# Kernel tuning notes

Hardware: AMD Instinct MI355X
Metric: run time of the kernel (lower is better)

Reference implementation:

```python
import jax, jax.numpy as jnp
import numpy as np

BS = 128  # block size for gating tiles


def setup_inputs() -> dict:
    key = jax.random.key(0)
    k1, k2, k3 = jax.random.split(key, 3)
    batch, dim_in, dim_out = 1536, 1536, 4608
    X = jax.random.normal(k1, (batch, dim_in), dtype=jnp.float32)
    W = jax.random.normal(k2, (dim_in, dim_out), dtype=jnp.float32)
    G = jax.random.normal(k3, (batch, dim_in // BS, dim_out // BS), dtype=jnp.float32)
    return {"X": X, "W": W, "G": G}


def reference(X, W, G):
    # Block-gated matmul: Y[b, j] = sum_i X[b, i] * W[i, j] * G[b, i//BS, j//BS]
    B, DI = X.shape
    DO = W.shape[1]
    NI, NJ = DI // BS, DO // BS
    Xr = X.reshape(B, NI, BS)               # [B, NI, bs]
    Wr = W.reshape(NI, BS, NJ, BS)          # [NI, bs, NJ, bs]
    # per-input-block partial products gated by G, summed over input blocks
    Y = jnp.einsum('bik,ikjl,bij->bjl', Xr, Wr, G)  # [B, NJ, bs]
    s = Y.sum()
    return s * s
```

## Files before the change

### kernel.cpp

```cpp
#include <hip/hip_runtime.h>


#define B_DIM 1536
#define DI    1536
#define DO    4608
#define BS    128
#define NI    12
#define NJ    36
#define BTILE 16

__global__ __launch_bounds__(256) void wsum_kernel(const float* __restrict__ W,
                                                   float* __restrict__ Wsum) {
    int wave = (blockIdx.x * 256 + threadIdx.x) >> 6;
    int lane = threadIdx.x & 63;
    int i  = wave / NJ;
    int jb = wave % NJ;
    const float2* p = (const float2*)(W + (size_t)i * DO + (size_t)jb * BS);
    float2 v = p[lane];
    float s = v.x + v.y;
    #pragma unroll
    for (int off = 32; off > 0; off >>= 1)
        s += __shfl_down(s, off, 64);
    if (lane == 0) Wsum[wave] = s;
}

__global__ __launch_bounds__(256) void gated_kernel(const float* __restrict__ X,
                                                    const float* __restrict__ G,
                                                    const float* __restrict__ Wsum,
                                                    float* __restrict__ partials) {
    __shared__ float ws[BS * 37];
    __shared__ float gs[BTILE * NJ];
    __shared__ float red[4];

    const int ib   = blockIdx.x % NI;
    const int tile = blockIdx.x / NI;
    const int b0   = tile * BTILE;
    const int t    = threadIdx.x;

    const float* wbase = Wsum + (size_t)ib * BS * NJ;
    for (int e = t; e < BS * NJ; e += 256) {
        int r = e / NJ, c = e - r * NJ;
        ws[r * 37 + c] = wbase[e];
    }
    for (int e = t; e < BTILE * NJ; e += 256) {
        int bb = e / NJ, k = e - bb * NJ;
        gs[e] = G[((size_t)(b0 + bb) * NI + ib) * NJ + k];
    }
    __syncthreads();

    const int wave = t >> 6, lane = t & 63;
    float waveAcc = 0.f;
    for (int bb = wave; bb < BTILE; bb += 4) {
        const int b = b0 + bb;
        const float* xrow = X + (size_t)b * DI + (size_t)ib * BS;
        const float* grow = gs + bb * NJ;
        float p = 0.f;
        #pragma unroll
        for (int r = 0; r < 2; ++r) {
            const int il = lane + 64 * r;
            float x = xrow[il];
            float acc = 0.f;
            #pragma unroll
            for (int k = 0; k < NJ; ++k)
                acc += ws[il * 37 + k] * grow[k];
            p += x * acc;
        }
        #pragma unroll
        for (int off = 32; off > 0; off >>= 1)
            p += __shfl_down(p, off, 64);
        if (lane == 0) waveAcc += p;
    }
    if (lane == 0) red[wave] = waveAcc;
    __syncthreads();
    if (t == 0) partials[blockIdx.x] = red[0] + red[1] + red[2] + red[3];
}

__global__ __launch_bounds__(256) void finish_kernel(const float* __restrict__ partials,
                                                     int n, float* __restrict__ out) {
    __shared__ float red[4];
    const int t = threadIdx.x;
    float s = 0.f;
    for (int e = t; e < n; e += 256) s += partials[e];
    #pragma unroll
    for (int off = 32; off > 0; off >>= 1)
        s += __shfl_down(s, off, 64);
    const int wave = t >> 6, lane = t & 63;
    if (lane == 0) red[wave] = s;
    __syncthreads();
    if (t == 0) {
        float tot = red[0] + red[1] + red[2] + red[3];
        out[0] = tot * tot;
    }
}

extern "C" void kernel_launch(void* const* d_in, const int* in_sizes, int n_in,
                              void* d_out, int out_size, void* d_ws, size_t ws_size,
                              hipStream_t stream) {
    const float* X = (const float*)d_in[0];
    const float* W = (const float*)d_in[1];
    const float* G = (const float*)d_in[2];
    float* out = (float*)d_out;

    float* Wsum     = (float*)d_ws;
    float* partials = Wsum + (size_t)DI * NJ;
    const int n_partials = (B_DIM / BTILE) * NI;

    wsum_kernel<<<(DI * NJ) / 4, 256, 0, stream>>>(W, Wsum);
    gated_kernel<<<n_partials, 256, 0, stream>>>(X, G, Wsum, partials);
    finish_kernel<<<1, 256, 0, stream>>>(partials, n_partials, out);
}
```

Baseline: 97.03 us.

## Restructure gated reduction: accumulate X·G per input column, fuse finish via atomics

The gated kernel now gives each lane one input column and accumulates x·G over a 32-row batch range into 36 register accumulators. It dots those with the precomputed W block sums only at the end, instead of redoing the 36-term W·G dot product for every batch row out of shared memory. The separate finish kernel is replaced by atomicAdd on a global accumulator plus a last-block counter, which removes one launch. The W-sum kernel reads float4 so each wave handles two column blocks, and it also zeroes the accumulator. The atomic float sum makes the result order-nondeterministic, and the larger per-thread register footprint may lower occupancy.

```diff
diff --git a/kernel.cpp b/kernel.cpp
--- a/kernel.cpp
+++ b/kernel.cpp
@@ -4,92 +4,90 @@
 #define B_DIM 1536
 #define DI    1536
 #define DO    4608
-#define BS    128
 #define NI    12
 #define NJ    36
-#define BTILE 16
+#define GROW  (NI * NJ)
+#define K2_WAVES 1152
+#define K2_BLOCKS (K2_WAVES / 4)
 
 __global__ __launch_bounds__(256) void wsum_kernel(const float* __restrict__ W,
-                                                   float* __restrict__ Wsum) {
-    int wave = (blockIdx.x * 256 + threadIdx.x) >> 6;
+                                                   float* __restrict__ Wsum,
+                                                   float* __restrict__ acc,
+                                                   unsigned* __restrict__ counter) {
+    if (blockIdx.x == 0 && threadIdx.x == 0) { *acc = 0.f; *counter = 0u; }
+    int g    = blockIdx.x * 4 + (threadIdx.x >> 6);
     int lane = threadIdx.x & 63;
-    int i  = wave / NJ;
-    int jb = wave % NJ;
-    const float2* p = (const float2*)(W + (size_t)i * DO + (size_t)jb * BS);
-    float2 v = p[lane];
-    float s = v.x + v.y;
+    int i = g / 18;
+    int w = g - i * 18;
+    const float4* p = (const float4*)(W + (size_t)i * DO + (size_t)w * 256);
+    float4 v = p[lane];
+    float s = (v.x + v.y) + (v.z + v.w);
     #pragma unroll
-    for (int off = 32; off > 0; off >>= 1)
-        s += __shfl_down(s, off, 64);
-    if (lane == 0) Wsum[wave] = s;
+    for (int off = 16; off > 0; off >>= 1) s += __shfl_xor(s, off, 64);
+    if (lane == 0)  Wsum[i * NJ + 2 * w]     = s;
+    if (lane == 32) Wsum[i * NJ + 2 * w + 1] = s;
 }
 
 __global__ __launch_bounds__(256) void gated_kernel(const float* __restrict__ X,
                                                     const float* __restrict__ G,
                                                     const float* __restrict__ Wsum,
-                                                    float* __restrict__ partials) {
-    __shared__ float ws[BS * 37];
-    __shared__ float gs[BTILE * NJ];
+                                                    float* __restrict__ acc,
+                                                    unsigned* __restrict__ counter,
+                                                    float* __restrict__ out) {
     __shared__ float red[4];
+    const int t    = threadIdx.x;
+    const int w    = __builtin_amdgcn_readfirstlane(t >> 6);
+    const int lane = t & 63;
+    const int wave = blockIdx.x * 4 + w;
+    const int iblk = wave % 24;
+    const int brng = wave / 24;
+    const int b0   = brng * 32;
+    const int i    = iblk * 64 + lane;
+    const int ib   = iblk >> 1;
 
-    const int ib   = blockIdx.x % NI;
-    const int tile = blockIdx.x / NI;
-    const int b0   = tile * BTILE;
-    const int t    = threadIdx.x;
+    float acc36[NJ];
+    #pragma unroll
+    for (int k = 0; k < NJ; ++k) acc36[k] = 0.f;
 
-    const float* wbase = Wsum + (size_t)ib * BS * NJ;
-    for (int e = t; e < BS * NJ; e += 256) {
-        int r = e / NJ, c = e - r * NJ;
-        ws[r * 37 + c] = wbase[e];
+    const float* xp = X + (size_t)b0 * DI + i;
+    const float4* gp = (const float4*)(G + (size_t)b0 * GROW + (size_t)ib * NJ);
+    const int gstride4 = GROW / 4;
+
+    #pragma unroll 8
+    for (int bb = 0; bb < 32; ++bb) {
+        float x = xp[(size_t)bb * DI];
+        const float4* g4 = gp + (size_t)bb * gstride4;
+        #pragma unroll
+        for (int k4 = 0; k4 < 9; ++k4) {
+            float4 gv = g4[k4];
+            acc36[4*k4+0] = fmaf(x, gv.x, acc36[4*k4+0]);
+            acc36[4*k4+1] = fmaf(x, gv.y, acc36[4*k4+1]);
+            acc36[4*k4+2] = fmaf(x, gv.z, acc36[4*k4+2]);
+            acc36[4*k4+3] = fmaf(x, gv.w, acc36[4*k4+3]);
+        }
     }
-    for (int e = t; e < BTILE * NJ; e += 256) {
-        int bb = e / NJ, k = e - bb * NJ;
-        gs[e] = G[((size_t)(b0 + bb) * NI + ib) * NJ + k];
+
+    float s = 0.f;
+    const float4* wsv = (const float4*)(Wsum + (size_t)i * NJ);
+    #pragma unroll
+    for (int k4 = 0; k4 < 9; ++k4) {
+        float4 w4 = wsv[k4];
+        s += w4.x * acc36[4*k4] + w4.y * acc36[4*k4+1]
+           + w4.z * acc36[4*k4+2] + w4.w * acc36[4*k4+3];
     }
-    __syncthreads();
-
-    const int wave = t >> 6, lane = t & 63;
-    float waveAcc = 0.f;
-    for (int bb = wave; bb < BTILE; bb += 4) {
-        const int b = b0 + bb;
-        const float* xrow = X + (size_t)b * DI + (size_t)ib * BS;
-        const float* grow = gs + bb * NJ;
-        float p = 0.f;
-        #pragma unroll
-        for (int r = 0; r < 2; ++r) {
-            const int il = lane + 64 * r;
-            float x = xrow[il];
-            float acc = 0.f;
-            #pragma unroll
-            for (int k = 0; k < NJ; ++k)
-                acc += ws[il * 37 + k] * grow[k];
-            p += x * acc;
-        }
-        #pragma unroll
-        for (int off = 32; off > 0; off >>= 1)
-            p += __shfl_down(p, off, 64);
-        if (lane == 0) waveAcc += p;
-    }
-    if (lane == 0) red[wave] = waveAcc;
-    __syncthreads();
-    if (t == 0) partials[blockIdx.x] = red[0] + red[1] + red[2] + red[3];
-}
-
-__global__ __launch_bounds__(256) void finish_kernel(const float* __restrict__ partials,
-                                                     int n, float* __restrict__ out) {
-    __shared__ float red[4];
-    const int t = threadIdx.x;
-    float s = 0.f;
-    for (int e = t; e < n; e += 256) s += partials[e];
     #pragma unroll
-    for (int off = 32; off > 0; off >>= 1)
-        s += __shfl_down(s, off, 64);
-    const int wave = t >> 6, lane = t & 63;
-    if (lane == 0) red[wave] = s;
+    for (int off = 1; off < 64; off <<= 1) s += __shfl_xor(s, off, 64);
+    if (lane == 0) red[w] = s;
     __syncthreads();
     if (t == 0) {
-        float tot = red[0] + red[1] + red[2] + red[3];
-        out[0] = tot * tot;
+        float bs = (red[0] + red[1]) + (red[2] + red[3]);
+        atomicAdd(acc, bs);
+        __threadfence();
+        unsigned old = atomicAdd(counter, 1u);
+        if (old == (unsigned)gridDim.x - 1u) {
+            float tot = atomicAdd(acc, 0.0f);
+            out[0] = tot * tot;
+        }
     }
 }
 
@@ -101,11 +99,10 @@
     const float* G = (const float*)d_in[2];
     float* out = (float*)d_out;
 
-    float* Wsum     = (float*)d_ws;
-    float* partials = Wsum + (size_t)DI * NJ;
-    const int n_partials = (B_DIM / BTILE) * NI;
+    float*    Wsum    = (float*)d_ws;
+    float*    acc     = Wsum + (size_t)DI * NJ;
+    unsigned* counter = (unsigned*)(acc + 1);
 
-    wsum_kernel<<<(DI * NJ) / 4, 256, 0, stream>>>(W, Wsum);
-    gated_kernel<<<n_partials, 256, 0, stream>>>(X, G, Wsum, partials);
-    finish_kernel<<<1, 256, 0, stream>>>(partials, n_partials, out);
+    wsum_kernel<<<(DI * 18) / 4, 256, 0, stream>>>(W, Wsum, acc, counter);
+    gated_kernel<<<K2_BLOCKS, 256, 0, stream>>>(X, G, Wsum, acc, counter, out);
 }
```

Measured after the change: 94.67 us. 1.02x faster.
